# Kernel optimization log

Measured on AMD Instinct MI355X. Metric: run time of the kernel, lower is better.

## Reference

```python
import jax, jax.numpy as jnp
import numpy as np

TEMPERATURE = 0.5
NEG_INF = -1e30  # mask value for diagonal in logsumexp (exact -inf also fine)


def _l2norm(x, eps=1e-12):
    # matches F.normalize(dim=1)
    n = jnp.sqrt(jnp.sum(x * x, axis=1, keepdims=True))
    return x / jnp.maximum(n, eps)


def setup_inputs() -> dict:
    key = jax.random.key(0)
    k1, k2, k3 = jax.random.split(key, 3)
    B, D, Q = 2048, 512, 32768
    return {
        "z_i": jax.random.normal(k1, (B, D), dtype=jnp.float32),
        "z_j": jax.random.normal(k2, (B, D), dtype=jnp.float32),
        "queue": jax.random.normal(k3, (Q, D), dtype=jnp.float32),
    }


def reference(z_i, z_j, queue):
    z = jnp.concatenate([z_i, z_j], axis=0)          # [N, D]
    N = z.shape[0]
    features = _l2norm(z)                            # [N, D]
    queue_norm = _l2norm(queue)                      # [Q, D]

    # NN retrieval from the support set
    sims_q = jnp.matmul(features, queue_norm.T)      # [N, Q]
    nn_idx = jnp.argmax(sims_q, axis=1)              # [N]
    nn_feats = queue_norm[nn_idx]                    # [N, D]

    # contrastive similarity between NNs and features
    sim = jnp.matmul(nn_feats, features.T) / TEMPERATURE  # [N, N]

    # positives: off-diagonals at +/- N//2
    sim_i_j = jnp.diagonal(sim, offset=N // 2)       # [N/2]
    sim_j_i = jnp.diagonal(sim, offset=-(N // 2))    # [N/2]
    positive_samples = jnp.concatenate([sim_i_j, sim_j_i], axis=0)  # [N]

    # negatives: all off-diagonal entries per row -> logsumexp with diag masked
    diag_mask = jnp.eye(N, dtype=bool)
    sim_masked = jnp.where(diag_mask, NEG_INF, sim)
    repulsion = jnp.mean(jax.scipy.special.logsumexp(sim_masked, axis=1))

    attraction = -jnp.mean(positive_samples)
    return attraction + repulsion
```

## Files before the change

### kernel.cpp

```cpp
#include <hip/hip_runtime.h>
#include <cstdint>

#define NFEAT 4096
#define NHALF 2048
#define DDIM  512
#define QROWS 32768

typedef unsigned short u16;
typedef unsigned char  u8;
typedef unsigned int   u32;
typedef unsigned long long u64;

typedef __bf16 bf16x8_t __attribute__((ext_vector_type(8)));
typedef float  f32x4_t  __attribute__((ext_vector_type(4)));
typedef float  f32x16_t __attribute__((ext_vector_type(16)));
typedef int    i32x4_t  __attribute__((ext_vector_type(4)));
typedef int    i32x8_t  __attribute__((ext_vector_type(8)));

typedef const __attribute__((address_space(1))) void* gas_ptr;
typedef __attribute__((address_space(3))) void* las_ptr;

__device__ __forceinline__ u16 f2bf(float f) {
  u32 u = __float_as_uint(f);
  u32 r = u + 0x7FFFu + ((u >> 16) & 1u);
  return (u16)(r >> 16);
}

__device__ __forceinline__ u32 fkey(float f) {
  u32 u = __float_as_uint(f);
  return (u & 0x80000000u) ? ~u : (u | 0x80000000u);
}

__global__ void k_norm(const float* __restrict__ zi, const float* __restrict__ zj,
                       const float* __restrict__ queue,
                       u16* __restrict__ featb, u16* __restrict__ queueb,
                       u8* __restrict__ feat8T, u8* __restrict__ queue8T) {
  int gw = (int)((blockIdx.x * blockDim.x + threadIdx.x) >> 6);
  int lane = threadIdx.x & 63;
  const float* src; u16* dst; u8* dstT; int r31;
  if (gw < NFEAT) {
    src = (gw < NHALF) ? (zi + (size_t)gw * DDIM) : (zj + (size_t)(gw - NHALF) * DDIM);
    dst = featb + (size_t)gw * DDIM;
    dstT = feat8T + (size_t)(gw >> 5) * 16384; r31 = gw & 31;
  } else {
    int r = gw - NFEAT;
    src = queue + (size_t)r * DDIM;
    dst = queueb + (size_t)r * DDIM;
    dstT = queue8T + (size_t)(r >> 5) * 16384; r31 = r & 31;
  }
  float4 v0 = reinterpret_cast<const float4*>(src)[lane * 2];
  float4 v1 = reinterpret_cast<const float4*>(src)[lane * 2 + 1];
  float ss = v0.x*v0.x + v0.y*v0.y + v0.z*v0.z + v0.w*v0.w
           + v1.x*v1.x + v1.y*v1.y + v1.z*v1.z + v1.w*v1.w;
  #pragma unroll
  for (int off = 32; off >= 1; off >>= 1) ss += __shfl_xor(ss, off);
  float inv = 1.0f / fmaxf(sqrtf(ss), 1e-12f);
  float n0 = v0.x*inv, n1 = v0.y*inv, n2 = v0.z*inv, n3 = v0.w*inv;
  float n4 = v1.x*inv, n5 = v1.y*inv, n6 = v1.z*inv, n7 = v1.w*inv;
  ushort4 o0, o1;
  o0.x = f2bf(n0); o0.y = f2bf(n1); o0.z = f2bf(n2); o0.w = f2bf(n3);
  o1.x = f2bf(n4); o1.y = f2bf(n5); o1.z = f2bf(n6); o1.w = f2bf(n7);
  reinterpret_cast<ushort4*>(dst)[lane * 2]     = o0;
  reinterpret_cast<ushort4*>(dst)[lane * 2 + 1] = o1;
  u32 p01, p23, p45, p67;
  asm("v_cvt_pk_fp8_f32 %0, %1, %2" : "=v"(p01) : "v"(n0), "v"(n1));
  asm("v_cvt_pk_fp8_f32 %0, %1, %2" : "=v"(p23) : "v"(n2), "v"(n3));
  asm("v_cvt_pk_fp8_f32 %0, %1, %2" : "=v"(p45) : "v"(n4), "v"(n5));
  asm("v_cvt_pk_fp8_f32 %0, %1, %2" : "=v"(p67) : "v"(n6), "v"(n7));
  uint2 w8;
  w8.x = (p01 & 0xFFFFu) | (p23 << 16);
  w8.y = (p45 & 0xFFFFu) | (p67 << 16);
  size_t toff = (size_t)(lane >> 3) * 2048 + ((lane >> 2) & 1) * 1024
              + ((lane >> 1) & 1) * 512 + r31 * 16 + (lane & 1) * 8;
  *reinterpret_cast<uint2*>(dstT + toff) = w8;
}

#define SB0() __builtin_amdgcn_sched_barrier(0)
#define LGKM0_SB() do { asm volatile("s_waitcnt lgkmcnt(0)" ::: "memory"); SB0(); } while (0)
#define LGKM8_SB() do { asm volatile("s_waitcnt lgkmcnt(8)" ::: "memory"); SB0(); } while (0)
#define VMCNT8() asm volatile("s_waitcnt vmcnt(8)" ::: "memory")
#define VMCNT4() asm volatile("s_waitcnt vmcnt(4)" ::: "memory")
#define VMCNT0() asm volatile("s_waitcnt vmcnt(0)" ::: "memory")
#define SBAR() __builtin_amdgcn_s_barrier()
#define RD(dst, base, off) asm volatile("ds_read_b128 %0, %1 offset:" off \
                                        : "=v"(dst) : "v"(base))

#define MFMA8(ACC, AV, BV) \
  ACC = __builtin_amdgcn_mfma_scale_f32_32x32x64_f8f6f4(AV, BV, ACC, 0, 0, 0, \
        0x7F7F7F7F, 0, 0x7F7F7F7F)

#define FP8_TILE(XA, XB) do { \
    i32x4_t a00, a01, a10, a11, b00, b01, b10, b11; \
    RD(a00, XA, "0"); RD(a01, XA, "512"); \
    RD(a10, XA, "2048"); RD(a11, XA, "2560"); \
    RD(b00, XB, "0"); RD(b01, XB, "512"); \
    RD(b10, XB, "2048"); RD(b11, XB, "2560"); \
    LGKM0_SB(); \
    i32x8_t A0 = __builtin_shufflevector(a00, a01, 0, 1, 2, 3, 4, 5, 6, 7); \
    i32x8_t A1 = __builtin_shufflevector(a10, a11, 0, 1, 2, 3, 4, 5, 6, 7); \
    i32x8_t B0 = __builtin_shufflevector(b00, b01, 0, 1, 2, 3, 4, 5, 6, 7); \
    i32x8_t B1 = __builtin_shufflevector(b10, b11, 0, 1, 2, 3, 4, 5, 6, 7); \
    __builtin_amdgcn_s_setprio(1); \
    MFMA8(acc00, A0, B0); \
    MFMA8(acc01, A0, B1); \
    MFMA8(acc10, A1, B0); \
    MFMA8(acc11, A1, B1); \
    __builtin_amdgcn_s_setprio(0); \
  } while (0)

__global__ __launch_bounds__(256, 2) void k_argmax_gemm8(
    const u8* __restrict__ feat8T, const u8* __restrict__ queue8T,
    u64* __restrict__ part) {
  __shared__ u8 lds[49152];
  const int tid = threadIdx.x;
  const int w = tid >> 6, lane = tid & 63;
  const int wr = w >> 1, wc = w & 1;
  const int l31 = lane & 31, hi = lane >> 5;
  const int bid = (int)blockIdx.x;
  const int wg = (bid & 7) * 1024 + (bid >> 3);
  const int mt = wg >> 5, ft = wg & 31;
  const int brow = mt * 128, bcol = ft * 128;

  const u8* pA = queue8T + (size_t)(brow >> 5) * 16384 + (tid >> 7) * 16384 + (tid & 127) * 16;
  const u8* pB = feat8T  + (size_t)(bcol >> 5) * 16384 + (tid >> 7) * 16384 + (tid & 127) * 16;
  const u32 dA = (u32)(size_t)(las_ptr)&lds[tid * 16];
  const u32 dB = dA + 8192;

  const u32 aAd = (u32)(size_t)(las_ptr)&lds[wr * 4096 + hi * 1024 + l31 * 16];
  const u32 bAd = (u32)(size_t)(las_ptr)&lds[8192 + wc * 4096 + hi * 1024 + l31 * 16];

  f32x16_t acc00 = {}, acc01 = {}, acc10 = {}, acc11 = {};

  auto stage = [&](int b, int t) {
    const u32 base = (u32)(b * 16384);
    __builtin_amdgcn_global_load_lds((gas_ptr)(pA + t * 2048),         (las_ptr)(size_t)(dA + base), 16, 0, 0);
    __builtin_amdgcn_global_load_lds((gas_ptr)(pA + 32768 + t * 2048), (las_ptr)(size_t)(dA + base + 4096), 16, 0, 0);
    __builtin_amdgcn_global_load_lds((gas_ptr)(pB + t * 2048),         (las_ptr)(size_t)(dB + base), 16, 0, 0);
    __builtin_amdgcn_global_load_lds((gas_ptr)(pB + 32768 + t * 2048), (las_ptr)(size_t)(dB + base + 4096), 16, 0, 0);
  };

  stage(0, 0); stage(1, 1);
  VMCNT4();
  SBAR();

  #pragma unroll
  for (int t = 0; t < 8; t++) {
    if (t <= 5) stage((t + 2) % 3, t + 2);
    const u32 bb = (u32)((t % 3) * 16384);
    FP8_TILE(aAd + bb, bAd + bb);
    if (t < 7) {
      if (t <= 5) VMCNT4(); else VMCNT0();
      SBAR();
    }
  }

  const int mslot = mt * 2 + wr;
  const int fbase = bcol + wc * 64 + l31;
  #pragma unroll
  for (int n = 0; n < 2; n++) {
    float bv = -3.0e38f; int br = 0;
    #pragma unroll
    for (int m = 0; m < 2; m++) {
      #pragma unroll
      for (int reg = 0; reg < 16; reg++) {
        float v = n == 0 ? (m == 0 ? acc00[reg] : acc10[reg])
                         : (m == 0 ? acc01[reg] : acc11[reg]);
        int lr = m * 32 + (reg & 3) + 8 * (reg >> 2);
        if (v > bv) { bv = v; br = lr; }
      }
    }
    u32 q = (u32)(brow + wr * 64 + br + 4 * hi);
    u64 key = ((u64)fkey(bv) << 32) | (u64)(0xFFFFFFFFu - q);
    u64 o = __shfl_xor(key, 32);
    key = key > o ? key : o;
    if (hi == 0) part[(size_t)(fbase + n * 32) * 512 + mslot] = key;
  }
}

__global__ void k_argmax_reduce(const u64* __restrict__ part, int* __restrict__ nnidx) {
  int row = (int)((blockIdx.x * blockDim.x + threadIdx.x) >> 6);
  int lane = threadIdx.x & 63;
  const u64* p = part + (size_t)row * 512;
  u64 best = 0;
  #pragma unroll
  for (int i = 0; i < 8; i++) { u64 v = p[lane * 8 + i]; best = best > v ? best : v; }
  #pragma unroll
  for (int off = 1; off < 64; off <<= 1) { u64 o = __shfl_xor(best, off); best = best > o ? best : o; }
  if (lane == 0) nnidx[row] = (int)(0xFFFFFFFFu - (u32)(best & 0xFFFFFFFFu));
}

#define MFMA_Q(MB, NB, AF, BF) do { \
  __builtin_amdgcn_s_setprio(1); \
  _Pragma("unroll") \
  for (int kk_ = 0; kk_ < 2; kk_++) \
    _Pragma("unroll") \
    for (int m_ = 0; m_ < 4; m_++) \
      _Pragma("unroll") \
      for (int n_ = 0; n_ < 2; n_++) \
        acc[MB + m_][NB + n_] = __builtin_amdgcn_mfma_f32_16x16x32_bf16( \
            AF[m_*2+kk_], BF[n_*2+kk_], acc[MB+m_][NB+n_], 0, 0, 0); \
  __builtin_amdgcn_s_setprio(0); } while (0)

#define ISSUE_G1(XA0, XA1, XB0, XB1) do { \
  RD(Bq[0],  XB0, "0");    RD(Bq[1],  XB1, "0");    \
  RD(Bq[2],  XB0, "2048"); RD(Bq[3],  XB1, "2048"); \
  RD(A03[0], XA0, "0");    RD(A03[1], XA1, "0");    \
  RD(A03[2], XA0, "2048"); RD(A03[3], XA1, "2048"); \
  RD(A03[4], XA0, "4096"); RD(A03[5], XA1, "4096"); \
  RD(A03[6], XA0, "6144"); RD(A03[7], XA1, "6144"); } while (0)

#define ISSUE_G2(XA0, XA1, XB0, XB1) do { \
  RD(Bq2[0], XB0, "4096");  RD(Bq2[1], XB1, "4096");  \
  RD(Bq2[2], XB0, "6144");  RD(Bq2[3], XB1, "6144");  \
  RD(A47[0], XA0, "8192");  RD(A47[1], XA1, "8192");  \
  RD(A47[2], XA0, "10240"); RD(A47[3], XA1, "10240"); \
  RD(A47[4], XA0, "12288"); RD(A47[5], XA1, "12288"); \
  RD(A47[6], XA0, "14336"); RD(A47[7], XA1, "14336"); } while (0)

#define GEMM_MAIN_LOOP() do { \
  stTile(0, 0); stTile(1, 1); \
  VMCNT8(); \
  SBAR(); SB0(); \
  { const u32 xA0 = aA0, xA1 = aA1, xB0 = bA0, xB1 = bA1; \
    ISSUE_G1(xA0, xA1, xB0, xB1); } \
  _Pragma("unroll") \
  for (int t = 0; t < 8; t++) { \
    const u32 bo  = (u32)((t & 1) * 65536); \
    const u32 obo = (u32)(((t + 1) & 1) * 65536); \
    const u32 xA0 = aA0 + bo,  xA1 = aA1 + bo,  xB0 = bA0 + bo,  xB1 = bA1 + bo; \
    const u32 yA0 = aA0 + obo, yA1 = aA1 + obo, yB0 = bA0 + obo, yB1 = bA1 + obo; \
    LGKM0_SB(); \
    ISSUE_G2(xA0, xA1, xB0, xB1); \
    SB0(); \
    MFMA_Q(0, 0, A03, Bq); \
    LGKM8_SB(); \
    MFMA_Q(0, 2, A03, Bq2); \
    LGKM0_SB(); \
    MFMA_Q(4, 0, A47, Bq); \
    VMCNT0(); \
    SBAR(); SB0(); \
    if (t < 7) { ISSUE_G1(yA0, yA1, yB0, yB1); } \
    if (t < 6) { stTile(t & 1, t + 2); } \
    SB0(); \
    MFMA_Q(4, 2, A47, Bq2); \
  } } while (0)

__global__ __launch_bounds__(512, 2) void k_sim_gemm(
    const u16* __restrict__ featb, const u16* __restrict__ queueb,
    const int* __restrict__ nnidx,
    float2* __restrict__ lsep, float* __restrict__ pos) {
  __shared__ u16 lds[65536];
  const int tid = threadIdx.x;
  const int w = tid >> 6, lane = tid & 63;
  const int wr = w >> 2, wc = w & 3;
  const int li = lane & 15, lg = lane >> 4;
  const int bid = (int)blockIdx.x;
  const int wg = (bid & 7) * 32 + (bid >> 3);
  const int mt = wg & 15, ct = wg >> 4;
  const int brow = mt * 256, bcol = ct * 256;

  const int srw = tid >> 3;
  const int ssl = (tid & 7) ^ ((tid >> 3) & 7);
  const int ldsw = w * 512;
  const u16* pA[4]; const u16* pB[4];
  #pragma unroll
  for (int h = 0; h < 2; h++)
    #pragma unroll
    for (int l = 0; l < 2; l++) {
      pA[h*2+l] = queueb + (size_t)nnidx[brow + h*128 + l*64 + srw] * DDIM + ssl * 8;
      pB[h*2+l] = featb  + (size_t)(bcol + h*128 + l*64 + srw) * DDIM + ssl * 8;
    }

  const int sx = li & 7;
  const int u0 = (lg ^ sx) * 8;
  const int u1 = ((4 + lg) ^ sx) * 8;
  const int aBase = wr * 8192 + li * 64;
  const int bBase = 16384 + (wc >> 1) * 8192 + ((wc & 1) * 64 + li) * 64;
  const u32 aA0 = (u32)(size_t)(las_ptr)&lds[aBase + u0];
  const u32 aA1 = (u32)(size_t)(las_ptr)&lds[aBase + u1];
  const u32 bA0 = (u32)(size_t)(las_ptr)&lds[bBase + u0];
  const u32 bA1 = (u32)(size_t)(las_ptr)&lds[bBase + u1];

  f32x4_t acc[8][4] = {};

  auto stTile = [&](int b, int t) {
    #pragma unroll
    for (int h = 0; h < 2; h++)
      #pragma unroll
      for (int l = 0; l < 2; l++)
        __builtin_amdgcn_global_load_lds((gas_ptr)(pA[h*2+l] + t * 64),
            (las_ptr)&lds[b * 32768 + h * 8192 + l * 4096 + ldsw], 16, 0, 0);
    #pragma unroll
    for (int h = 0; h < 2; h++)
      #pragma unroll
      for (int l = 0; l < 2; l++)
        __builtin_amdgcn_global_load_lds((gas_ptr)(pB[h*2+l] + t * 64),
            (las_ptr)&lds[b * 32768 + 16384 + h * 8192 + l * 4096 + ldsw], 16, 0, 0);
  };

  bf16x8_t A03[8], A47[8], Bq[4], Bq2[4];

  GEMM_MAIN_LOOP();

  #pragma unroll
  for (int m = 0; m < 8; m++) {
    #pragma unroll
    for (int j = 0; j < 4; j++) {
      int row = brow + wr * 128 + m * 16 + lg * 4 + j;
      float vals[4];
      float vmax = -3.0e38f;
      #pragma unroll
      for (int n = 0; n < 4; n++) {
        int col = bcol + wc * 64 + n * 16 + li;
        float v = acc[m][n][j] * 2.0f;
        if (col == (row ^ NHALF)) pos[row] = v;
        if (col == row) v = -1.0e30f;
        vals[n] = v;
        vmax = fmaxf(vmax, v);
      }
      float sum = 0.f;
      #pragma unroll
      for (int n = 0; n < 4; n++) sum += __expf(vals[n] - vmax);
      #pragma unroll
      for (int off = 1; off < 16; off <<= 1) {
        float mo = __shfl_xor(vmax, off);
        float so = __shfl_xor(sum, off);
        float M = fmaxf(vmax, mo);
        sum = sum * __expf(vmax - M) + so * __expf(mo - M);
        vmax = M;
      }
      if (li == 0) lsep[(size_t)row * 64 + (ct * 4 + wc)] = make_float2(vmax, sum);
    }
  }
}

__global__ void k_lse(const float2* __restrict__ lsep, float* __restrict__ lse) {
  int row = (int)((blockIdx.x * blockDim.x + threadIdx.x) >> 6);
  int lane = threadIdx.x & 63;
  float2 p = lsep[(size_t)row * 64 + lane];
  float m = p.x, s = p.y;
  #pragma unroll
  for (int off = 1; off < 64; off <<= 1) {
    float mo = __shfl_xor(m, off), so = __shfl_xor(s, off);
    float M = fmaxf(m, mo);
    s = s * __expf(m - M) + so * __expf(mo - M);
    m = M;
  }
  if (lane == 0) lse[row] = m + __logf(s);
}

__global__ void k_final(const float* __restrict__ lse, const float* __restrict__ pos,
                        float* __restrict__ out) {
  __shared__ float red[4];
  int tid = threadIdx.x;
  float a = 0.f;
  for (int i = tid; i < NFEAT; i += 256) a += lse[i] - pos[i];
  #pragma unroll
  for (int off = 32; off >= 1; off >>= 1) a += __shfl_xor(a, off);
  if ((tid & 63) == 0) red[tid >> 6] = a;
  __syncthreads();
  if (tid == 0) out[0] = (red[0] + red[1] + red[2] + red[3]) / (float)NFEAT;
}

extern "C" void kernel_launch(void* const* d_in, const int* in_sizes, int n_in,
                              void* d_out, int out_size, void* d_ws, size_t ws_size,
                              hipStream_t stream) {
  const float* zi    = (const float*)d_in[0];
  const float* zj    = (const float*)d_in[1];
  const float* queue = (const float*)d_in[2];
  float* out = (float*)d_out;
  char* ws = (char*)d_ws;

  u16*    queueb  = (u16*)(ws + 0);
  u16*    featb   = (u16*)(ws + 33554432);
  u8*     queue8T = (u8*)(ws + 37748736);
  u8*     feat8T  = (u8*)(ws + 54525952);
  u64*    part    = (u64*)(ws + 56623104);
  int*    nnidx   = (int*)(ws + 73400320);
  float2* lsep    = (float2*)(ws + 73416704);
  float*  pos     = (float*)(ws + 75513856);
  float*  lse     = (float*)(ws + 75530240);

  k_norm<<<9216, 256, 0, stream>>>(zi, zj, queue, featb, queueb, feat8T, queue8T);
  k_argmax_gemm8<<<8192, 256, 0, stream>>>(feat8T, queue8T, part);
  k_argmax_reduce<<<1024, 256, 0, stream>>>(part, nnidx);
  k_sim_gemm<<<256, 512, 0, stream>>>(featb, queueb, nnidx, lsep, pos);
  k_lse<<<1024, 256, 0, stream>>>(lsep, lse);
  k_final<<<1, 256, 0, stream>>>(lse, pos, out);
}
```

Before: 131.8 us.

## Deepen LDS ring to four stages and double-buffer register fragments for MFMA

Grows the shared-memory ring from three to four 16 KB stages and issues three global-to-LDS prefetches up front. The next tile's LDS reads go into a second register set while the current tile's scaled FP8 MFMAs run, using a partial lgkmcnt wait instead of a full drain. The aim is to hide LDS read latency behind matrix math and keep more global loads in flight. In exchange it uses more LDS per block and more registers, which could hurt occupancy, and the K loop has only eight steps, which limits how much overlap the pipeline can reach.

```diff
diff --git a/kernel.cpp b/kernel.cpp
--- a/kernel.cpp
+++ b/kernel.cpp
@@ -89,29 +89,28 @@
   ACC = __builtin_amdgcn_mfma_scale_f32_32x32x64_f8f6f4(AV, BV, ACC, 0, 0, 0, \
         0x7F7F7F7F, 0, 0x7F7F7F7F)
 
-#define FP8_TILE(XA, XB) do { \
-    i32x4_t a00, a01, a10, a11, b00, b01, b10, b11; \
-    RD(a00, XA, "0"); RD(a01, XA, "512"); \
-    RD(a10, XA, "2048"); RD(a11, XA, "2560"); \
-    RD(b00, XB, "0"); RD(b01, XB, "512"); \
-    RD(b10, XB, "2048"); RD(b11, XB, "2560"); \
-    LGKM0_SB(); \
-    i32x8_t A0 = __builtin_shufflevector(a00, a01, 0, 1, 2, 3, 4, 5, 6, 7); \
-    i32x8_t A1 = __builtin_shufflevector(a10, a11, 0, 1, 2, 3, 4, 5, 6, 7); \
-    i32x8_t B0 = __builtin_shufflevector(b00, b01, 0, 1, 2, 3, 4, 5, 6, 7); \
-    i32x8_t B1 = __builtin_shufflevector(b10, b11, 0, 1, 2, 3, 4, 5, 6, 7); \
+#define FP8_READ(P, XA, XB) do { \
+    RD(P##a00, XA, "0"); RD(P##a01, XA, "512"); \
+    RD(P##a10, XA, "2048"); RD(P##a11, XA, "2560"); \
+    RD(P##b00, XB, "0"); RD(P##b01, XB, "512"); \
+    RD(P##b10, XB, "2048"); RD(P##b11, XB, "2560"); } while (0)
+
+#define FP8_MFMA(P) do { \
+    i32x8_t A0 = __builtin_shufflevector(P##a00, P##a01, 0, 1, 2, 3, 4, 5, 6, 7); \
+    i32x8_t A1 = __builtin_shufflevector(P##a10, P##a11, 0, 1, 2, 3, 4, 5, 6, 7); \
+    i32x8_t B0 = __builtin_shufflevector(P##b00, P##b01, 0, 1, 2, 3, 4, 5, 6, 7); \
+    i32x8_t B1 = __builtin_shufflevector(P##b10, P##b11, 0, 1, 2, 3, 4, 5, 6, 7); \
     __builtin_amdgcn_s_setprio(1); \
     MFMA8(acc00, A0, B0); \
     MFMA8(acc01, A0, B1); \
     MFMA8(acc10, A1, B0); \
     MFMA8(acc11, A1, B1); \
-    __builtin_amdgcn_s_setprio(0); \
-  } while (0)
+    __builtin_amdgcn_s_setprio(0); } while (0)
 
 __global__ __launch_bounds__(256, 2) void k_argmax_gemm8(
     const u8* __restrict__ feat8T, const u8* __restrict__ queue8T,
     u64* __restrict__ part) {
-  __shared__ u8 lds[49152];
+  __shared__ u8 lds[65536];
   const int tid = threadIdx.x;
   const int w = tid >> 6, lane = tid & 63;
   const int wr = w >> 1, wc = w & 1;
@@ -130,6 +129,8 @@
   const u32 bAd = (u32)(size_t)(las_ptr)&lds[8192 + wc * 4096 + hi * 1024 + l31 * 16];
 
   f32x16_t acc00 = {}, acc01 = {}, acc10 = {}, acc11 = {};
+  i32x4_t p_a00, p_a01, p_a10, p_a11, p_b00, p_b01, p_b10, p_b11;
+  i32x4_t q_a00, q_a01, q_a10, q_a11, q_b00, q_b01, q_b10, q_b11;
 
   auto stage = [&](int b, int t) {
     const u32 base = (u32)(b * 16384);
@@ -139,19 +140,23 @@
     __builtin_amdgcn_global_load_lds((gas_ptr)(pB + 32768 + t * 2048), (las_ptr)(size_t)(dB + base + 4096), 16, 0, 0);
   };
 
-  stage(0, 0); stage(1, 1);
+  stage(0, 0); stage(1, 1); stage(2, 2);
   VMCNT4();
   SBAR();
+  FP8_READ(p_, aAd, bAd);
 
   #pragma unroll
   for (int t = 0; t < 8; t++) {
-    if (t <= 5) stage((t + 2) % 3, t + 2);
-    const u32 bb = (u32)((t % 3) * 16384);
-    FP8_TILE(aAd + bb, bAd + bb);
+    const u32 nb = (u32)(((t + 1) & 3) * 16384);
     if (t < 7) {
-      if (t <= 5) VMCNT4(); else VMCNT0();
-      SBAR();
+      if ((t & 1) == 0) FP8_READ(q_, aAd + nb, bAd + nb);
+      else              FP8_READ(p_, aAd + nb, bAd + nb);
     }
+    if (t <= 4) stage((t + 3) & 3, t + 3);
+    if (t < 7) LGKM8_SB(); else LGKM0_SB();
+    if ((t & 1) == 0) FP8_MFMA(p_); else FP8_MFMA(q_);
+    if (t <= 4)      { VMCNT4(); SBAR(); }
+    else if (t == 5) { VMCNT0(); SBAR(); }
   }
 
   const int mslot = mt * 2 + wr;
```

After: 133.9 us. About the same (+1.5%).

## Run similarity GEMM in FP8 and drop bf16 copies of normalized features

Applied to the files above, without the earlier changes.

The second GEMM (NN features times features, followed by the logsumexp epilogue) now uses the FP8 transposed buffers and the same 32x32x64 scaled-MFMA pipeline as the argmax GEMM, gathering NN rows straight from queue8T. The bf16 normalized copies of the queue and features are no longer written, which removes a large global-memory store from k_norm. The sim GEMM switches to 128x128 tiles with 1024 blocks of 256 threads, and its epilogue writes per-column partial (max, sum) pairs for 64 row slots. The tradeoff is FP8 precision in the logits divided by temperature, which may affect the accuracy of the loss.

```diff
diff --git a/kernel.cpp b/kernel.cpp
--- a/kernel.cpp
+++ b/kernel.cpp
@@ -11,8 +11,6 @@
 typedef unsigned int   u32;
 typedef unsigned long long u64;
 
-typedef __bf16 bf16x8_t __attribute__((ext_vector_type(8)));
-typedef float  f32x4_t  __attribute__((ext_vector_type(4)));
 typedef float  f32x16_t __attribute__((ext_vector_type(16)));
 typedef int    i32x4_t  __attribute__((ext_vector_type(4)));
 typedef int    i32x8_t  __attribute__((ext_vector_type(8)));
@@ -20,12 +18,6 @@
 typedef const __attribute__((address_space(1))) void* gas_ptr;
 typedef __attribute__((address_space(3))) void* las_ptr;
 
-__device__ __forceinline__ u16 f2bf(float f) {
-  u32 u = __float_as_uint(f);
-  u32 r = u + 0x7FFFu + ((u >> 16) & 1u);
-  return (u16)(r >> 16);
-}
-
 __device__ __forceinline__ u32 fkey(float f) {
   u32 u = __float_as_uint(f);
   return (u & 0x80000000u) ? ~u : (u | 0x80000000u);
@@ -33,19 +25,16 @@
 
 __global__ void k_norm(const float* __restrict__ zi, const float* __restrict__ zj,
                        const float* __restrict__ queue,
-                       u16* __restrict__ featb, u16* __restrict__ queueb,
                        u8* __restrict__ feat8T, u8* __restrict__ queue8T) {
   int gw = (int)((blockIdx.x * blockDim.x + threadIdx.x) >> 6);
   int lane = threadIdx.x & 63;
-  const float* src; u16* dst; u8* dstT; int r31;
+  const float* src; u8* dstT; int r31;
   if (gw < NFEAT) {
     src = (gw < NHALF) ? (zi + (size_t)gw * DDIM) : (zj + (size_t)(gw - NHALF) * DDIM);
-    dst = featb + (size_t)gw * DDIM;
     dstT = feat8T + (size_t)(gw >> 5) * 16384; r31 = gw & 31;
   } else {
     int r = gw - NFEAT;
     src = queue + (size_t)r * DDIM;
-    dst = queueb + (size_t)r * DDIM;
     dstT = queue8T + (size_t)(r >> 5) * 16384; r31 = r & 31;
   }
   float4 v0 = reinterpret_cast<const float4*>(src)[lane * 2];
@@ -57,11 +46,6 @@
   float inv = 1.0f / fmaxf(sqrtf(ss), 1e-12f);
   float n0 = v0.x*inv, n1 = v0.y*inv, n2 = v0.z*inv, n3 = v0.w*inv;
   float n4 = v1.x*inv, n5 = v1.y*inv, n6 = v1.z*inv, n7 = v1.w*inv;
-  ushort4 o0, o1;
-  o0.x = f2bf(n0); o0.y = f2bf(n1); o0.z = f2bf(n2); o0.w = f2bf(n3);
-  o1.x = f2bf(n4); o1.y = f2bf(n5); o1.z = f2bf(n6); o1.w = f2bf(n7);
-  reinterpret_cast<ushort4*>(dst)[lane * 2]     = o0;
-  reinterpret_cast<ushort4*>(dst)[lane * 2 + 1] = o1;
   u32 p01, p23, p45, p67;
   asm("v_cvt_pk_fp8_f32 %0, %1, %2" : "=v"(p01) : "v"(n0), "v"(n1));
   asm("v_cvt_pk_fp8_f32 %0, %1, %2" : "=v"(p23) : "v"(n2), "v"(n3));
@@ -77,8 +61,6 @@
 
 #define SB0() __builtin_amdgcn_sched_barrier(0)
 #define LGKM0_SB() do { asm volatile("s_waitcnt lgkmcnt(0)" ::: "memory"); SB0(); } while (0)
-#define LGKM8_SB() do { asm volatile("s_waitcnt lgkmcnt(8)" ::: "memory"); SB0(); } while (0)
-#define VMCNT8() asm volatile("s_waitcnt vmcnt(8)" ::: "memory")
 #define VMCNT4() asm volatile("s_waitcnt vmcnt(4)" ::: "memory")
 #define VMCNT0() asm volatile("s_waitcnt vmcnt(0)" ::: "memory")
 #define SBAR() __builtin_amdgcn_s_barrier()
@@ -108,6 +90,21 @@
     __builtin_amdgcn_s_setprio(0); \
   } while (0)
 
+#define FP8_MAIN_LOOP() do { \
+  stage(0, 0); stage(1, 1); \
+  VMCNT4(); \
+  SBAR(); \
+  _Pragma("unroll") \
+  for (int t = 0; t < 8; t++) { \
+    if (t <= 5) stage((t + 2) % 3, t + 2); \
+    const u32 bb = (u32)((t % 3) * 16384); \
+    FP8_TILE(aAd + bb, bAd + bb); \
+    if (t < 7) { \
+      if (t <= 5) VMCNT4(); else VMCNT0(); \
+      SBAR(); \
+    } \
+  } } while (0)
+
 __global__ __launch_bounds__(256, 2) void k_argmax_gemm8(
     const u8* __restrict__ feat8T, const u8* __restrict__ queue8T,
     u64* __restrict__ part) {
@@ -139,20 +136,7 @@
     __builtin_amdgcn_global_load_lds((gas_ptr)(pB + 32768 + t * 2048), (las_ptr)(size_t)(dB + base + 4096), 16, 0, 0);
   };
 
-  stage(0, 0); stage(1, 1);
-  VMCNT4();
-  SBAR();
-
-  #pragma unroll
-  for (int t = 0; t < 8; t++) {
-    if (t <= 5) stage((t + 2) % 3, t + 2);
-    const u32 bb = (u32)((t % 3) * 16384);
-    FP8_TILE(aAd + bb, bAd + bb);
-    if (t < 7) {
-      if (t <= 5) VMCNT4(); else VMCNT0();
-      SBAR();
-    }
-  }
+  FP8_MAIN_LOOP();
 
   const int mslot = mt * 2 + wr;
   const int fbase = bcol + wc * 64 + l31;
@@ -189,148 +173,80 @@
   if (lane == 0) nnidx[row] = (int)(0xFFFFFFFFu - (u32)(best & 0xFFFFFFFFu));
 }
 
-#define MFMA_Q(MB, NB, AF, BF) do { \
-  __builtin_amdgcn_s_setprio(1); \
-  _Pragma("unroll") \
-  for (int kk_ = 0; kk_ < 2; kk_++) \
-    _Pragma("unroll") \
-    for (int m_ = 0; m_ < 4; m_++) \
-      _Pragma("unroll") \
-      for (int n_ = 0; n_ < 2; n_++) \
-        acc[MB + m_][NB + n_] = __builtin_amdgcn_mfma_f32_16x16x32_bf16( \
-            AF[m_*2+kk_], BF[n_*2+kk_], acc[MB+m_][NB+n_], 0, 0, 0); \
-  __builtin_amdgcn_s_setprio(0); } while (0)
-
-#define ISSUE_G1(XA0, XA1, XB0, XB1) do { \
-  RD(Bq[0],  XB0, "0");    RD(Bq[1],  XB1, "0");    \
-  RD(Bq[2],  XB0, "2048"); RD(Bq[3],  XB1, "2048"); \
-  RD(A03[0], XA0, "0");    RD(A03[1], XA1, "0");    \
-  RD(A03[2], XA0, "2048"); RD(A03[3], XA1, "2048"); \
-  RD(A03[4], XA0, "4096"); RD(A03[5], XA1, "4096"); \
-  RD(A03[6], XA0, "6144"); RD(A03[7], XA1, "6144"); } while (0)
-
-#define ISSUE_G2(XA0, XA1, XB0, XB1) do { \
-  RD(Bq2[0], XB0, "4096");  RD(Bq2[1], XB1, "4096");  \
-  RD(Bq2[2], XB0, "6144");  RD(Bq2[3], XB1, "6144");  \
-  RD(A47[0], XA0, "8192");  RD(A47[1], XA1, "8192");  \
-  RD(A47[2], XA0, "10240"); RD(A47[3], XA1, "10240"); \
-  RD(A47[4], XA0, "12288"); RD(A47[5], XA1, "12288"); \
-  RD(A47[6], XA0, "14336"); RD(A47[7], XA1, "14336"); } while (0)
-
-#define GEMM_MAIN_LOOP() do { \
-  stTile(0, 0); stTile(1, 1); \
-  VMCNT8(); \
-  SBAR(); SB0(); \
-  { const u32 xA0 = aA0, xA1 = aA1, xB0 = bA0, xB1 = bA1; \
-    ISSUE_G1(xA0, xA1, xB0, xB1); } \
-  _Pragma("unroll") \
-  for (int t = 0; t < 8; t++) { \
-    const u32 bo  = (u32)((t & 1) * 65536); \
-    const u32 obo = (u32)(((t + 1) & 1) * 65536); \
-    const u32 xA0 = aA0 + bo,  xA1 = aA1 + bo,  xB0 = bA0 + bo,  xB1 = bA1 + bo; \
-    const u32 yA0 = aA0 + obo, yA1 = aA1 + obo, yB0 = bA0 + obo, yB1 = bA1 + obo; \
-    LGKM0_SB(); \
-    ISSUE_G2(xA0, xA1, xB0, xB1); \
-    SB0(); \
-    MFMA_Q(0, 0, A03, Bq); \
-    LGKM8_SB(); \
-    MFMA_Q(0, 2, A03, Bq2); \
-    LGKM0_SB(); \
-    MFMA_Q(4, 0, A47, Bq); \
-    VMCNT0(); \
-    SBAR(); SB0(); \
-    if (t < 7) { ISSUE_G1(yA0, yA1, yB0, yB1); } \
-    if (t < 6) { stTile(t & 1, t + 2); } \
-    SB0(); \
-    MFMA_Q(4, 2, A47, Bq2); \
-  } } while (0)
-
-__global__ __launch_bounds__(512, 2) void k_sim_gemm(
-    const u16* __restrict__ featb, const u16* __restrict__ queueb,
+__global__ __launch_bounds__(256, 2) void k_sim_gemm8(
+    const u8* __restrict__ feat8T, const u8* __restrict__ queue8T,
     const int* __restrict__ nnidx,
     float2* __restrict__ lsep, float* __restrict__ pos) {
-  __shared__ u16 lds[65536];
+  __shared__ u8 lds[49152];
   const int tid = threadIdx.x;
   const int w = tid >> 6, lane = tid & 63;
-  const int wr = w >> 2, wc = w & 3;
-  const int li = lane & 15, lg = lane >> 4;
+  const int wr = w >> 1, wc = w & 1;
+  const int l31 = lane & 31, hi = lane >> 5;
   const int bid = (int)blockIdx.x;
-  const int wg = (bid & 7) * 32 + (bid >> 3);
-  const int mt = wg & 15, ct = wg >> 4;
-  const int brow = mt * 256, bcol = ct * 256;
-
-  const int srw = tid >> 3;
-  const int ssl = (tid & 7) ^ ((tid >> 3) & 7);
-  const int ldsw = w * 512;
-  const u16* pA[4]; const u16* pB[4];
-  #pragma unroll
-  for (int h = 0; h < 2; h++)
+  const int wg = (bid & 7) * 128 + (bid >> 3);
+  const int mt = wg >> 5, nt = wg & 31;
+  const int mtb = mt * 128, ntb = nt * 128;
+
+  const u8* pA = feat8T + (size_t)(mtb >> 5) * 16384 + (tid >> 7) * 16384 + (tid & 127) * 16;
+  const int g0 = nnidx[ntb + (tid >> 7) * 32 + (tid & 31)];
+  const int g1 = nnidx[ntb + (tid >> 7) * 32 + 64 + (tid & 31)];
+  const int sub = ((tid >> 6) & 1) * 1024 + ((tid >> 5) & 1) * 512;
+  const u8* pB0 = queue8T + (size_t)(g0 >> 5) * 16384 + sub + (g0 & 31) * 16;
+  const u8* pB1 = queue8T + (size_t)(g1 >> 5) * 16384 + sub + (g1 & 31) * 16;
+  const u32 dA = (u32)(size_t)(las_ptr)&lds[tid * 16];
+  const u32 dB = dA + 8192;
+
+  const u32 aAd = (u32)(size_t)(las_ptr)&lds[wr * 4096 + hi * 1024 + l31 * 16];
+  const u32 bAd = (u32)(size_t)(las_ptr)&lds[8192 + wc * 4096 + hi * 1024 + l31 * 16];
+
+  f32x16_t acc00 = {}, acc01 = {}, acc10 = {}, acc11 = {};
+
+  auto stage = [&](int b, int t) {
+    const u32 base = (u32)(b * 16384);
+    __builtin_amdgcn_global_load_lds((gas_ptr)(pA + t * 2048),         (las_ptr)(size_t)(dA + base), 16, 0, 0);
+    __builtin_amdgcn_global_load_lds((gas_ptr)(pA + 32768 + t * 2048), (las_ptr)(size_t)(dA + base + 4096), 16, 0, 0);
+    __builtin_amdgcn_global_load_lds((gas_ptr)(pB0 + t * 2048),        (las_ptr)(size_t)(dB + base), 16, 0, 0);
+    __builtin_amdgcn_global_load_lds((gas_ptr)(pB1 + t * 2048),        (las_ptr)(size_t)(dB + base + 4096), 16, 0, 0);
+  };
+
+  FP8_MAIN_LOOP();
+
+  const int mslot = mt * 2 + wr;
+  const int ibase = mtb + wr * 64 + 4 * hi;
+  #pragma unroll
+  for (int n = 0; n < 2; n++) {
+    const int j = ntb + wc * 64 + n * 32 + l31;
+    const int jp = j ^ NHALF;
+    float mx = -3.0e38f;
     #pragma unroll
-    for (int l = 0; l < 2; l++) {
-      pA[h*2+l] = queueb + (size_t)nnidx[brow + h*128 + l*64 + srw] * DDIM + ssl * 8;
-      pB[h*2+l] = featb  + (size_t)(bcol + h*128 + l*64 + srw) * DDIM + ssl * 8;
+    for (int m = 0; m < 2; m++) {
+      #pragma unroll
+      for (int reg = 0; reg < 16; reg++) {
+        float v = (n == 0 ? (m == 0 ? acc00[reg] : acc10[reg])
+                          : (m == 0 ? acc01[reg] : acc11[reg])) * 2.0f;
+        int i = ibase + m * 32 + (reg & 3) + 8 * (reg >> 2);
+        if (i == jp) pos[j] = v;
+        if (i == j) v = -1.0e30f;
+        mx = fmaxf(mx, v);
+      }
     }
-
-  const int sx = li & 7;
-  const int u0 = (lg ^ sx) * 8;
-  const int u1 = ((4 + lg) ^ sx) * 8;
-  const int aBase = wr * 8192 + li * 64;
-  const int bBase = 16384 + (wc >> 1) * 8192 + ((wc & 1) * 64 + li) * 64;
-  const u32 aA0 = (u32)(size_t)(las_ptr)&lds[aBase + u0];
-  const u32 aA1 = (u32)(size_t)(las_ptr)&lds[aBase + u1];
-  const u32 bA0 = (u32)(size_t)(las_ptr)&lds[bBase + u0];
-  const u32 bA1 = (u32)(size_t)(las_ptr)&lds[bBase + u1];
-
-  f32x4_t acc[8][4] = {};
-
-  auto stTile = [&](int b, int t) {
+    float sm = 0.f;
     #pragma unroll
-    for (int h = 0; h < 2; h++)
+    for (int m = 0; m < 2; m++) {
       #pragma unroll
-      for (int l = 0; l < 2; l++)
-        __builtin_amdgcn_global_load_lds((gas_ptr)(pA[h*2+l] + t * 64),
-            (las_ptr)&lds[b * 32768 + h * 8192 + l * 4096 + ldsw], 16, 0, 0);
-    #pragma unroll
-    for (int h = 0; h < 2; h++)
-      #pragma unroll
-      for (int l = 0; l < 2; l++)
-        __builtin_amdgcn_global_load_lds((gas_ptr)(pB[h*2+l] + t * 64),
-            (las_ptr)&lds[b * 32768 + 16384 + h * 8192 + l * 4096 + ldsw], 16, 0, 0);
-  };
-
-  bf16x8_t A03[8], A47[8], Bq[4], Bq2[4];
-
-  GEMM_MAIN_LOOP();
-
-  #pragma unroll
-  for (int m = 0; m < 8; m++) {
-    #pragma unroll
-    for (int j = 0; j < 4; j++) {
-      int row = brow + wr * 128 + m * 16 + lg * 4 + j;
-      float vals[4];
-      float vmax = -3.0e38f;
-      #pragma unroll
-      for (int n = 0; n < 4; n++) {
-        int col = bcol + wc * 64 + n * 16 + li;
-        float v = acc[m][n][j] * 2.0f;
-        if (col == (row ^ NHALF)) pos[row] = v;
-        if (col == row) v = -1.0e30f;
-        vals[n] = v;
-        vmax = fmaxf(vmax, v);
+      for (int reg = 0; reg < 16; reg++) {
+        float v = (n == 0 ? (m == 0 ? acc00[reg] : acc10[reg])
+                          : (m == 0 ? acc01[reg] : acc11[reg])) * 2.0f;
+        int i = ibase + m * 32 + (reg & 3) + 8 * (reg >> 2);
+        if (i == j) v = -1.0e30f;
+        sm += __expf(v - mx);
       }
-      float sum = 0.f;
-      #pragma unroll
-      for (int n = 0; n < 4; n++) sum += __expf(vals[n] - vmax);
-      #pragma unroll
-      for (int off = 1; off < 16; off <<= 1) {
-        float mo = __shfl_xor(vmax, off);
-        float so = __shfl_xor(sum, off);
-        float M = fmaxf(vmax, mo);
-        sum = sum * __expf(vmax - M) + so * __expf(mo - M);
-        vmax = M;
-      }
-      if (li == 0) lsep[(size_t)row * 64 + (ct * 4 + wc)] = make_float2(vmax, sum);
     }
+    float mo = __shfl_xor(mx, 32);
+    float so = __shfl_xor(sm, 32);
+    float M = fmaxf(mx, mo);
+    sm = sm * __expf(mx - M) + so * __expf(mo - M);
+    if (hi == 0) lsep[(size_t)j * 64 + mslot] = make_float2(M, sm);
   }
 }
 
@@ -371,20 +287,18 @@
   float* out = (float*)d_out;
   char* ws = (char*)d_ws;
 
-  u16*    queueb  = (u16*)(ws + 0);
-  u16*    featb   = (u16*)(ws + 33554432);
-  u8*     queue8T = (u8*)(ws + 37748736);
-  u8*     feat8T  = (u8*)(ws + 54525952);
-  u64*    part    = (u64*)(ws + 56623104);
-  int*    nnidx   = (int*)(ws + 73400320);
-  float2* lsep    = (float2*)(ws + 73416704);
-  float*  pos     = (float*)(ws + 75513856);
-  float*  lse     = (float*)(ws + 75530240);
-
-  k_norm<<<9216, 256, 0, stream>>>(zi, zj, queue, featb, queueb, feat8T, queue8T);
+  u8*     queue8T = (u8*)(ws + 0);
+  u8*     feat8T  = (u8*)(ws + 16777216);
+  u64*    part    = (u64*)(ws + 18874368);
+  int*    nnidx   = (int*)(ws + 35651584);
+  float2* lsep    = (float2*)(ws + 35667968);
+  float*  pos     = (float*)(ws + 37765120);
+  float*  lse     = (float*)(ws + 37781504);
+
+  k_norm<<<9216, 256, 0, stream>>>(zi, zj, queue, feat8T, queue8T);
   k_argmax_gemm8<<<8192, 256, 0, stream>>>(feat8T, queue8T, part);
   k_argmax_reduce<<<1024, 256, 0, stream>>>(part, nnidx);
-  k_sim_gemm<<<256, 512, 0, stream>>>(featb, queueb, nnidx, lsep, pos);
+  k_sim_gemm8<<<1024, 256, 0, stream>>>(feat8T, queue8T, nnidx, lsep, pos);
   k_lse<<<1024, 256, 0, stream>>>(lsep, lse);
   k_final<<<1, 256, 0, stream>>>(lse, pos, out);
 }
```

Measured after the change: 144.4 us. 1.1x slower.
